# Optimization experiments

Hardware: AMD Instinct MI355X
Metric: run time of the kernel (lower is better)

The kernel has to match this reference:

```python
import jax, jax.numpy as jnp
import numpy as np

EMBED_DIM = 1024
NUM_HEADS = 16
HEAD_DIM = EMBED_DIM // NUM_HEADS
B, N = 4, 2048


def setup_inputs() -> dict:
    key = jax.random.key(0)
    k = jax.random.split(key, 5)
    s = 1.0 / np.sqrt(EMBED_DIM)
    return {
        "x": jax.random.normal(k[0], (B, N, EMBED_DIM), dtype=jnp.float32),
        "W_qkv": jax.random.uniform(k[1], (EMBED_DIM, 3 * EMBED_DIM), jnp.float32, -s, s),
        "b_qkv": jax.random.uniform(k[2], (3 * EMBED_DIM,), jnp.float32, -s, s),
        "W_proj": jax.random.uniform(k[3], (EMBED_DIM, EMBED_DIM), jnp.float32, -s, s),
        "b_proj": jax.random.uniform(k[4], (EMBED_DIM,), jnp.float32, -s, s),
    }


def reference(x, W_qkv, b_qkv, W_proj, b_proj):
    b, n, c = x.shape
    qkv = x @ W_qkv + b_qkv                       # [B,N,3C]
    qkv = qkv.reshape(b, n, 3, NUM_HEADS, HEAD_DIM)
    q = qkv[:, :, 0].transpose(0, 2, 1, 3)        # [B,H,N,D]
    k = qkv[:, :, 1].transpose(0, 2, 1, 3)
    v = qkv[:, :, 2].transpose(0, 2, 1, 3)
    scale = 1.0 / np.sqrt(HEAD_DIM).astype(np.float32)
    scores = jnp.einsum("bhqd,bhkd->bhqk", q, k) * scale
    attn = jax.nn.softmax(scores, axis=-1)
    out = jnp.einsum("bhqk,bhkd->bhqd", attn, v)  # [B,H,N,D]
    out = out.transpose(0, 2, 1, 3).reshape(b, n, c)
    return out @ W_proj + b_proj
```

## Files before the change

### kernel.cpp

```cpp
#include <hip/hip_runtime.h>
#include <math.h>


typedef __bf16 bf16x8 __attribute__((ext_vector_type(8)));
typedef float f32x4 __attribute__((ext_vector_type(4)));

#define EMBED 1024
#define NHEAD 16
#define BATCH 4
#define SEQ 2048
#define M_TOT 8192
#define QKV_N 3072
#define QSCALE 0.18033688011112042f

__device__ __forceinline__ ushort f2bf(float f) {
  union { float f; unsigned u; } x; x.f = f;
  unsigned r = x.u + 0x7FFFu + ((x.u >> 16) & 1u);
  return (ushort)(r >> 16);
}

__device__ __forceinline__ uint cvt2bf(float a, float b) {
#if __has_builtin(__builtin_amdgcn_cvt_pk_bf16_f32)
  typedef __bf16 bf16x2 __attribute__((ext_vector_type(2)));
  union { bf16x2 v; uint u; } c;
  c.v = __builtin_amdgcn_cvt_pk_bf16_f32(a, b);
  return c.u;
#else
  return (uint)f2bf(a) | ((uint)f2bf(b) << 16);
#endif
}

__device__ __forceinline__ f32x4 mfma16(bf16x8 a, bf16x8 b, f32x4 c) {
  return __builtin_amdgcn_mfma_f32_16x16x32_bf16(a, b, c, 0, 0, 0);
}

__device__ __forceinline__ void gl2lds16(const void* g, void* l) {
  __builtin_amdgcn_global_load_lds(
      (const __attribute__((address_space(1))) unsigned int*)g,
      (__attribute__((address_space(3))) unsigned int*)l, 16, 0, 0);
}

__global__ __launch_bounds__(256) void cvt_f32_bf16(
    const float* __restrict__ in, ushort* __restrict__ out) {
  int i = (blockIdx.x * 256 + threadIdx.x) * 4;
  float4 v = *reinterpret_cast<const float4*>(&in[i]);
  uint2 w = {cvt2bf(v.x, v.y), cvt2bf(v.z, v.w)};
  *reinterpret_cast<uint2*>(&out[i]) = w;
}

__global__ __launch_bounds__(256) void transpose_to_bf16(
    const float* __restrict__ in, ushort* __restrict__ out, int Kd, int Nd) {
  __shared__ float tile[64][65];
  const int t = threadIdx.x;
  const int n0 = blockIdx.x * 64, k0 = blockIdx.y * 64;
#pragma unroll
  for (int i = 0; i < 16; ++i) {
    int e = t + 256 * i;
    int kr = e >> 6, nc = e & 63;
    tile[kr][nc] = in[(size_t)(k0 + kr) * Nd + n0 + nc];
  }
  __syncthreads();
#pragma unroll
  for (int i = 0; i < 16; ++i) {
    int e = t + 256 * i;
    int nr = e >> 6, kc = e & 63;
    out[(size_t)(n0 + nr) * Kd + k0 + kc] = f2bf(tile[kc][nr]);
  }
}

__global__ __launch_bounds__(256) void gemm_bf16(
    const ushort* __restrict__ A, const ushort* __restrict__ Bt,
    const float* __restrict__ bias, void* __restrict__ Cout,
    ushort* __restrict__ vtgout, int M, int N, int K, int mode) {
  __shared__ ushort As[128 * 32];
  __shared__ ushort Bs[128 * 32];
  const int t = threadIdx.x;
  const int wave = t >> 6, lane = t & 63;
  const int lane15 = lane & 15, quad = lane >> 4;
  const int m0 = blockIdx.y * 128, n0 = blockIdx.x * 128;
  const int wm = (wave >> 1) * 64, wn = (wave & 1) * 64;

  int srow[2], scol[2], sdst[2];
#pragma unroll
  for (int j = 0; j < 2; ++j) {
    int c = (j * 4 + wave) * 64 + lane;
    int row = c >> 2;
    scol[j] = (((c & 3) ^ ((row >> 1) & 3)) * 8);
    srow[j] = row;
    sdst[j] = (j * 4 + wave) * 512;
  }
  const int swG = (lane15 >> 1) & 3;

  f32x4 acc[4][4] = {};

  for (int k0 = 0; k0 < K; k0 += 32) {
#pragma unroll
    for (int j = 0; j < 2; ++j) {
      gl2lds16(&A[(size_t)(m0 + srow[j]) * K + k0 + scol[j]], &As[sdst[j]]);
      gl2lds16(&Bt[(size_t)(n0 + srow[j]) * K + k0 + scol[j]], &Bs[sdst[j]]);
    }
    __syncthreads();

    bf16x8 af[4], bfr[4];
#pragma unroll
    for (int ms = 0; ms < 4; ++ms)
      af[ms] = *reinterpret_cast<const bf16x8*>(
          &As[(wm + ms * 16 + lane15) * 32 + ((quad ^ swG) * 8)]);
#pragma unroll
    for (int ns = 0; ns < 4; ++ns)
      bfr[ns] = *reinterpret_cast<const bf16x8*>(
          &Bs[(wn + ns * 16 + lane15) * 32 + ((quad ^ swG) * 8)]);
#pragma unroll
    for (int ms = 0; ms < 4; ++ms)
#pragma unroll
      for (int ns = 0; ns < 4; ++ns)
        acc[ms][ns] = mfma16(af[ms], bfr[ns], acc[ms][ns]);
    __syncthreads();
  }

  if (mode == 0) {
    float* out = (float*)Cout;
#pragma unroll
    for (int ns = 0; ns < 4; ++ns) {
      int col = n0 + wn + ns * 16 + lane15;
      float bv = bias[col];
#pragma unroll
      for (int ms = 0; ms < 4; ++ms)
#pragma unroll
        for (int r = 0; r < 4; ++r) {
          int row = m0 + wm + ms * 16 + quad * 4 + r;
          out[(size_t)row * N + col] = acc[ms][ns][r] + bv;
        }
    }
  } else {
    ushort* qk = (ushort*)Cout;
#pragma unroll
    for (int ns = 0; ns < 4; ++ns) {
      int col = n0 + wn + ns * 16 + lane15;
      float bv = bias[col];
      if (col < 2048) {
        float sc = (col < 1024) ? QSCALE : 1.0f;
#pragma unroll
        for (int ms = 0; ms < 4; ++ms) {
          int row = m0 + wm + ms * 16 + quad * 4;
          uint u01 = cvt2bf((acc[ms][ns][0] + bv) * sc, (acc[ms][ns][1] + bv) * sc);
          uint u23 = cvt2bf((acc[ms][ns][2] + bv) * sc, (acc[ms][ns][3] + bv) * sc);
          qk[(size_t)(row + 0) * 2048 + col] = (ushort)u01;
          qk[(size_t)(row + 1) * 2048 + col] = (ushort)(u01 >> 16);
          qk[(size_t)(row + 2) * 2048 + col] = (ushort)u23;
          qk[(size_t)(row + 3) * 2048 + col] = (ushort)(u23 >> 16);
        }
      } else {
        int dp = col - 2048;
#pragma unroll
        for (int ms = 0; ms < 4; ++ms) {
          int row = m0 + wm + ms * 16 + quad * 4;
          int b = row >> 11, seq = row & 2047;
          uint2 w = {cvt2bf(acc[ms][ns][0] + bv, acc[ms][ns][1] + bv),
                     cvt2bf(acc[ms][ns][2] + bv, acc[ms][ns][3] + bv)};
          *reinterpret_cast<uint2*>(
              &vtgout[((size_t)(b * 1024 + dp) << 11) + seq]) = w;
        }
      }
    }
  }
}

#define APD 72

__global__ __launch_bounds__(256) void attn_kernel(
    const ushort* __restrict__ qk, const ushort* __restrict__ vtg,
    ushort* __restrict__ out) {
  __shared__ ushort Ks[2][4096];
  __shared__ ushort Vt[2][4096];
  __shared__ ushort Ps[4 * 16 * APD];

  const int t = threadIdx.x;
  const int wave = t >> 6, lane = t & 63;
  const int lane15 = lane & 15, quad = lane >> 4;
  const int qt = blockIdx.x, h = blockIdx.y, b = blockIdx.z;
  const size_t boff = (size_t)b * SEQ * 2048;

  int sdst[2];
  const ushort* kptr[2];
  const ushort* vptr[2];
#pragma unroll
  for (int j = 0; j < 2; ++j) {
    int lg = (j * 4 + wave) * 64 + lane;
    int row = lg >> 3;
    int col = ((lg & 7) ^ (row & 7)) * 8;
    sdst[j] = (j * 4 + wave) * 512;
    kptr[j] = qk + boff + (size_t)row * 2048 + 1024 + h * 64 + col;
    vptr[j] = vtg + ((size_t)(b * 1024 + h * 64 + row) << 11) + col;
  }

  bf16x8 qf[2];
  {
    size_t qoff = boff + (size_t)(qt * 64 + wave * 16 + lane15) * 2048 + h * 64;
    qf[0] = *reinterpret_cast<const bf16x8*>(&qk[qoff + quad * 8]);
    qf[1] = *reinterpret_cast<const bf16x8*>(&qk[qoff + 32 + quad * 8]);
  }

  bf16x8 ones;
#pragma unroll
  for (int j = 0; j < 8; ++j) ones[j] = (__bf16)1.0f;

  f32x4 O[4] = {};
  f32x4 lacc = {};
  const int sw = lane15 & 7;
  const int pbase = wave * 16 * APD;

#pragma unroll
  for (int j = 0; j < 2; ++j) {
    gl2lds16(kptr[j], &Ks[0][sdst[j]]);
    gl2lds16(vptr[j], &Vt[0][sdst[j]]);
  }
  __syncthreads();

  for (int kt = 0; kt < SEQ / 64; ++kt) {
    const int cur = kt & 1, nxt = cur ^ 1;
    const int ktn = (kt < SEQ / 64 - 1) ? kt + 1 : kt;
#pragma unroll
    for (int j = 0; j < 2; ++j) {
      gl2lds16(kptr[j] + (size_t)ktn * 64 * 2048, &Ks[nxt][sdst[j]]);
      gl2lds16(vptr[j] + ktn * 64, &Vt[nxt][sdst[j]]);
    }

    f32x4 st[4];
#pragma unroll
    for (int nsub = 0; nsub < 4; ++nsub) {
      const int kr = (nsub * 16 + lane15) * 64;
      bf16x8 kf0 = *reinterpret_cast<const bf16x8*>(
          &Ks[cur][kr + ((quad ^ sw) * 8)]);
      bf16x8 kf1 = *reinterpret_cast<const bf16x8*>(
          &Ks[cur][kr + (((quad + 4) ^ sw) * 8)]);
      f32x4 a = {-32.0f, -32.0f, -32.0f, -32.0f};
      a = mfma16(kf0, qf[0], a);
      a = mfma16(kf1, qf[1], a);
      st[nsub] = a;
    }

#pragma unroll
    for (int nsub = 0; nsub < 4; ++nsub) {
      uint2 w = {cvt2bf(exp2f(st[nsub][0]), exp2f(st[nsub][1])),
                 cvt2bf(exp2f(st[nsub][2]), exp2f(st[nsub][3]))};
      *reinterpret_cast<uint2*>(
          &Ps[pbase + lane15 * APD + nsub * 16 + quad * 4]) = w;
    }

#pragma unroll
    for (int kk = 0; kk < 2; ++kk) {
      bf16x8 pf = *reinterpret_cast<const bf16x8*>(
          &Ps[pbase + lane15 * APD + kk * 32 + quad * 8]);
#pragma unroll
      for (int dsub = 0; dsub < 4; ++dsub) {
        int d = dsub * 16 + lane15;
        bf16x8 vf = *reinterpret_cast<const bf16x8*>(
            &Vt[cur][d * 64 + (((kk * 4 + quad) ^ sw) * 8)]);
        O[dsub] = mfma16(pf, vf, O[dsub]);
      }
      lacc = mfma16(pf, ones, lacc);
    }
    __syncthreads();
  }

#pragma unroll
  for (int r = 0; r < 4; ++r) {
    float linv = __builtin_amdgcn_rcpf(lacc[r]);
    size_t rowoff =
        (size_t)(b * SEQ + qt * 64 + wave * 16 + quad * 4 + r) * EMBED + h * 64;
    uint u01 = cvt2bf(O[0][r] * linv, O[1][r] * linv);
    uint u23 = cvt2bf(O[2][r] * linv, O[3][r] * linv);
    out[rowoff + 0 * 16 + lane15] = (ushort)u01;
    out[rowoff + 1 * 16 + lane15] = (ushort)(u01 >> 16);
    out[rowoff + 2 * 16 + lane15] = (ushort)u23;
    out[rowoff + 3 * 16 + lane15] = (ushort)(u23 >> 16);
  }
}

extern "C" void kernel_launch(void* const* d_in, const int* in_sizes, int n_in,
                              void* d_out, int out_size, void* d_ws,
                              size_t ws_size, hipStream_t stream) {
  const float* x = (const float*)d_in[0];
  const float* Wqkv = (const float*)d_in[1];
  const float* bqkv = (const float*)d_in[2];
  const float* Wproj = (const float*)d_in[3];
  const float* bproj = (const float*)d_in[4];
  float* out = (float*)d_out;

  char* ws = (char*)d_ws;
  ushort* Wqkv_t = (ushort*)ws;
  ushort* Wproj_t = (ushort*)(ws + 6291456);
  ushort* qk = (ushort*)(ws + 8388608);
  ushort* vtg = (ushort*)(ws + 41943040);
  ushort* xb = (ushort*)(ws + 58720256);
  ushort* attnout = (ushort*)(ws + 58720256);

  cvt_f32_bf16<<<M_TOT * EMBED / 1024, 256, 0, stream>>>(x, xb);
  transpose_to_bf16<<<dim3(QKV_N / 64, EMBED / 64), 256, 0, stream>>>(
      Wqkv, Wqkv_t, EMBED, QKV_N);
  transpose_to_bf16<<<dim3(EMBED / 64, EMBED / 64), 256, 0, stream>>>(
      Wproj, Wproj_t, EMBED, EMBED);
  gemm_bf16<<<dim3(QKV_N / 128, M_TOT / 128), 256, 0, stream>>>(
      xb, Wqkv_t, bqkv, qk, vtg, M_TOT, QKV_N, EMBED, 1);
  attn_kernel<<<dim3(SEQ / 64, NHEAD, BATCH), 256, 0, stream>>>(
      qk, vtg, attnout);
  gemm_bf16<<<dim3(EMBED / 128, M_TOT / 128), 256, 0, stream>>>(
      attnout, Wproj_t, bproj, out, nullptr, M_TOT, EMBED, EMBED, 0);
}
```

Before: 353.4 us.

## Process four query tiles per attention block to reuse K/V tiles

Each attention block now handles 256 query rows (four 64-row groups) instead of 64. It loads each K/V tile into LDS once and holds the K and V fragments in registers across all four groups, which cuts global and LDS traffic for K/V by four times. The grid is reordered so batch-head is the fast dimension, and the launch bounds request 2 blocks per SM. In exchange, register pressure rises sharply (4x accumulators and fragments), the grid shrinks from 2048 to 512 blocks, and occupancy may drop.

```diff
diff --git a/kernel.cpp b/kernel.cpp
--- a/kernel.cpp
+++ b/kernel.cpp
@@ -167,18 +167,20 @@
 }
 
 #define APD 72
-
-__global__ __launch_bounds__(256) void attn_kernel(
+#define QG 4
+
+__global__ __launch_bounds__(256, 2) void attn_kernel(
     const ushort* __restrict__ qk, const ushort* __restrict__ vtg,
     ushort* __restrict__ out) {
   __shared__ ushort Ks[2][4096];
   __shared__ ushort Vt[2][4096];
-  __shared__ ushort Ps[4 * 16 * APD];
+  __shared__ ushort Ps[4][16 * APD];
 
   const int t = threadIdx.x;
   const int wave = t >> 6, lane = t & 63;
   const int lane15 = lane & 15, quad = lane >> 4;
-  const int qt = blockIdx.x, h = blockIdx.y, b = blockIdx.z;
+  const int bh = blockIdx.x, qg = blockIdx.y;
+  const int b = bh >> 4, h = bh & 15;
   const size_t boff = (size_t)b * SEQ * 2048;
 
   int sdst[2];
@@ -194,21 +196,23 @@
     vptr[j] = vtg + ((size_t)(b * 1024 + h * 64 + row) << 11) + col;
   }
 
-  bf16x8 qf[2];
-  {
-    size_t qoff = boff + (size_t)(qt * 64 + wave * 16 + lane15) * 2048 + h * 64;
-    qf[0] = *reinterpret_cast<const bf16x8*>(&qk[qoff + quad * 8]);
-    qf[1] = *reinterpret_cast<const bf16x8*>(&qk[qoff + 32 + quad * 8]);
+  bf16x8 qf[QG][2];
+#pragma unroll
+  for (int g = 0; g < QG; ++g) {
+    size_t qoff =
+        boff + (size_t)(qg * 256 + g * 64 + wave * 16 + lane15) * 2048 + h * 64;
+    qf[g][0] = *reinterpret_cast<const bf16x8*>(&qk[qoff + quad * 8]);
+    qf[g][1] = *reinterpret_cast<const bf16x8*>(&qk[qoff + 32 + quad * 8]);
   }
 
   bf16x8 ones;
 #pragma unroll
   for (int j = 0; j < 8; ++j) ones[j] = (__bf16)1.0f;
 
-  f32x4 O[4] = {};
-  f32x4 lacc = {};
+  f32x4 O[QG][4] = {};
+  f32x4 lacc[QG] = {};
   const int sw = lane15 & 7;
-  const int pbase = wave * 16 * APD;
+  ushort* ps = Ps[wave];
 
 #pragma unroll
   for (int j = 0; j < 2; ++j) {
@@ -219,63 +223,77 @@
 
   for (int kt = 0; kt < SEQ / 64; ++kt) {
     const int cur = kt & 1, nxt = cur ^ 1;
-    const int ktn = (kt < SEQ / 64 - 1) ? kt + 1 : kt;
-#pragma unroll
-    for (int j = 0; j < 2; ++j) {
-      gl2lds16(kptr[j] + (size_t)ktn * 64 * 2048, &Ks[nxt][sdst[j]]);
-      gl2lds16(vptr[j] + ktn * 64, &Vt[nxt][sdst[j]]);
-    }
-
-    f32x4 st[4];
+    if (kt < SEQ / 64 - 1) {
+#pragma unroll
+      for (int j = 0; j < 2; ++j) {
+        gl2lds16(kptr[j] + (size_t)(kt + 1) * 64 * 2048, &Ks[nxt][sdst[j]]);
+        gl2lds16(vptr[j] + (kt + 1) * 64, &Vt[nxt][sdst[j]]);
+      }
+    }
+
+    bf16x8 kf[4][2], vf[2][4];
 #pragma unroll
     for (int nsub = 0; nsub < 4; ++nsub) {
       const int kr = (nsub * 16 + lane15) * 64;
-      bf16x8 kf0 = *reinterpret_cast<const bf16x8*>(
+      kf[nsub][0] = *reinterpret_cast<const bf16x8*>(
           &Ks[cur][kr + ((quad ^ sw) * 8)]);
-      bf16x8 kf1 = *reinterpret_cast<const bf16x8*>(
+      kf[nsub][1] = *reinterpret_cast<const bf16x8*>(
           &Ks[cur][kr + (((quad + 4) ^ sw) * 8)]);
-      f32x4 a = {-32.0f, -32.0f, -32.0f, -32.0f};
-      a = mfma16(kf0, qf[0], a);
-      a = mfma16(kf1, qf[1], a);
-      st[nsub] = a;
-    }
-
-#pragma unroll
-    for (int nsub = 0; nsub < 4; ++nsub) {
-      uint2 w = {cvt2bf(exp2f(st[nsub][0]), exp2f(st[nsub][1])),
-                 cvt2bf(exp2f(st[nsub][2]), exp2f(st[nsub][3]))};
-      *reinterpret_cast<uint2*>(
-          &Ps[pbase + lane15 * APD + nsub * 16 + quad * 4]) = w;
-    }
-
-#pragma unroll
-    for (int kk = 0; kk < 2; ++kk) {
-      bf16x8 pf = *reinterpret_cast<const bf16x8*>(
-          &Ps[pbase + lane15 * APD + kk * 32 + quad * 8]);
+    }
+#pragma unroll
+    for (int kk = 0; kk < 2; ++kk)
 #pragma unroll
       for (int dsub = 0; dsub < 4; ++dsub) {
         int d = dsub * 16 + lane15;
-        bf16x8 vf = *reinterpret_cast<const bf16x8*>(
+        vf[kk][dsub] = *reinterpret_cast<const bf16x8*>(
             &Vt[cur][d * 64 + (((kk * 4 + quad) ^ sw) * 8)]);
-        O[dsub] = mfma16(pf, vf, O[dsub]);
-      }
-      lacc = mfma16(pf, ones, lacc);
+      }
+
+#pragma unroll
+    for (int g = 0; g < QG; ++g) {
+      f32x4 st[4];
+#pragma unroll
+      for (int nsub = 0; nsub < 4; ++nsub) {
+        f32x4 a = {-32.0f, -32.0f, -32.0f, -32.0f};
+        a = mfma16(kf[nsub][0], qf[g][0], a);
+        a = mfma16(kf[nsub][1], qf[g][1], a);
+        st[nsub] = a;
+      }
+#pragma unroll
+      for (int nsub = 0; nsub < 4; ++nsub) {
+        uint2 w = {cvt2bf(exp2f(st[nsub][0]), exp2f(st[nsub][1])),
+                   cvt2bf(exp2f(st[nsub][2]), exp2f(st[nsub][3]))};
+        *reinterpret_cast<uint2*>(
+            &ps[lane15 * APD + nsub * 16 + quad * 4]) = w;
+      }
+#pragma unroll
+      for (int kk = 0; kk < 2; ++kk) {
+        bf16x8 pf = *reinterpret_cast<const bf16x8*>(
+            &ps[lane15 * APD + kk * 32 + quad * 8]);
+#pragma unroll
+        for (int dsub = 0; dsub < 4; ++dsub)
+          O[g][dsub] = mfma16(pf, vf[kk][dsub], O[g][dsub]);
+        lacc[g] = mfma16(pf, ones, lacc[g]);
+      }
     }
     __syncthreads();
   }
 
 #pragma unroll
-  for (int r = 0; r < 4; ++r) {
-    float linv = __builtin_amdgcn_rcpf(lacc[r]);
-    size_t rowoff =
-        (size_t)(b * SEQ + qt * 64 + wave * 16 + quad * 4 + r) * EMBED + h * 64;
-    uint u01 = cvt2bf(O[0][r] * linv, O[1][r] * linv);
-    uint u23 = cvt2bf(O[2][r] * linv, O[3][r] * linv);
-    out[rowoff + 0 * 16 + lane15] = (ushort)u01;
-    out[rowoff + 1 * 16 + lane15] = (ushort)(u01 >> 16);
-    out[rowoff + 2 * 16 + lane15] = (ushort)u23;
-    out[rowoff + 3 * 16 + lane15] = (ushort)(u23 >> 16);
-  }
+  for (int g = 0; g < QG; ++g)
+#pragma unroll
+    for (int r = 0; r < 4; ++r) {
+      float linv = __builtin_amdgcn_rcpf(lacc[g][r]);
+      size_t rowoff =
+          (size_t)(b * SEQ + qg * 256 + g * 64 + wave * 16 + quad * 4 + r) *
+              EMBED + h * 64;
+      uint u01 = cvt2bf(O[g][0][r] * linv, O[g][1][r] * linv);
+      uint u23 = cvt2bf(O[g][2][r] * linv, O[g][3][r] * linv);
+      out[rowoff + 0 * 16 + lane15] = (ushort)u01;
+      out[rowoff + 1 * 16 + lane15] = (ushort)(u01 >> 16);
+      out[rowoff + 2 * 16 + lane15] = (ushort)u23;
+      out[rowoff + 3 * 16 + lane15] = (ushort)(u23 >> 16);
+    }
 }
 
 extern "C" void kernel_launch(void* const* d_in, const int* in_sizes, int n_in,
@@ -303,7 +321,7 @@
       Wproj, Wproj_t, EMBED, EMBED);
   gemm_bf16<<<dim3(QKV_N / 128, M_TOT / 128), 256, 0, stream>>>(
       xb, Wqkv_t, bqkv, qk, vtg, M_TOT, QKV_N, EMBED, 1);
-  attn_kernel<<<dim3(SEQ / 64, NHEAD, BATCH), 256, 0, stream>>>(
+  attn_kernel<<<dim3(NHEAD * BATCH, SEQ / 256), 256, 0, stream>>>(
       qk, vtg, attnout);
   gemm_bf16<<<dim3(EMBED / 128, M_TOT / 128), 256, 0, stream>>>(
       attnout, Wproj_t, bproj, out, nullptr, M_TOT, EMBED, EMBED, 0);
```

Measured after the change: 314.1 us. -11.1%, faster.
